# Kernel tuning notes

Hardware: AMD Instinct MI355X
Metric: run time of the kernel (lower is better)

## Reference

```python
import jax, jax.numpy as jnp
import numpy as np

B, L, P = 16, 128, 8192
ALPHA = 2.0            # current_alpha (softness_start)
STEP_PROGRESS = 0.5    # > 0.15 so e_ghost == 0; t_gate = sigmoid(3.0)
PROT_RADII = np.array([1.7, 1.55, 1.52, 1.8], dtype=np.float32)
PROT_EPS = np.array([0.1, 0.1, 0.15, 0.2], dtype=np.float32)
VDW_RADII = np.array([1.7, 1.55, 1.52, 1.8, 1.1, 1.47, 1.75, 1.85, 1.98], dtype=np.float32)
EPSILON = np.array([0.086, 0.17, 0.21, 0.25, 0.015, 0.061, 0.265, 0.32, 0.4], dtype=np.float32)


def setup_inputs() -> dict:
    key = jax.random.key(0)
    ks = jax.random.split(key, 6)
    # positions spread over ~ a binding-pocket-sized box so distances are realistic
    pos_L = jax.random.normal(ks[0], (B, L, 3), jnp.float32) * 8.0
    pos_P = jax.random.normal(ks[1], (B, P, 3), jnp.float32) * 8.0
    q_L = jax.random.normal(ks[2], (B, L), jnp.float32) * 0.3
    q_P = jax.random.normal(ks[3], (B, P), jnp.float32) * 0.3
    x_L = jax.random.uniform(ks[4], (B, L, 9), jnp.float32)
    x_L = x_L / jnp.sum(x_L, axis=-1, keepdims=True)  # type probabilities
    x_P = jax.random.uniform(ks[5], (B, P, 4), jnp.float32)
    x_P = x_P / jnp.sum(x_P, axis=-1, keepdims=True)
    return {
        'pos_L': pos_L, 'pos_P': pos_P, 'q_L': q_L, 'q_P': q_P,
        'x_L': x_L, 'x_P': x_P,
        'vdw_radii': jnp.asarray(VDW_RADII), 'epsilon_tbl': jnp.asarray(EPSILON),
    }


def reference(pos_L, pos_P, q_L, q_P, x_L, x_P, vdw_radii, epsilon_tbl):
    sg = jax.lax.stop_gradient
    # pairwise geometry: diff [B,L,P,3]
    diff = pos_L[:, :, None, :] - pos_P[:, None, :, :]
    dist_sq = jnp.sum(diff * diff, axis=-1)              # [B,L,P]
    dist = jnp.sqrt(dist_sq + 1e-8)
    # mixed vdw radii
    type_probs_L = x_L[..., :9]
    radii_L = type_probs_L @ vdw_radii                    # [B,L]
    radii_P = x_P[..., :4] @ jnp.asarray(PROT_RADII)      # [B,P]
    sigma_ij = radii_L[:, :, None] + radii_P[:, None, :]  # [B,L,P]
    # soft-core distance
    soft_dist = jnp.sqrt(dist_sq + ALPHA * sigma_ij * sigma_ij + 1e-8)
    # electrostatics (dielectric = 4.0), tanh-clamped
    e_elec_raw = 332.06 * q_L[:, :, None] * q_P[:, None, :] / (4.0 * soft_dist)
    e_elec = 200.0 * jnp.tanh(e_elec_raw / 200.0)
    # LJ 12-6 with geometric-mean epsilon
    eps_L = jax.nn.relu(type_probs_L @ epsilon_tbl)       # [B,L]
    eps_P = x_P[..., :4] @ jnp.asarray(PROT_EPS)          # [B,P]
    eps_ij = jnp.sqrt(eps_L[:, :, None] * eps_P[:, None, :] + 1e-8)
    ratio = jnp.minimum(sigma_ij / (soft_dist + 1e-8), 5.0)
    ratio6 = ratio ** 6
    ratio12 = ratio6 * ratio6
    e_vdw_raw = 4.0 * eps_ij * (ratio12 - ratio6)
    e_pos = 500.0 * jnp.tanh(jax.nn.relu(e_vdw_raw) / 500.0)
    e_neg = -10.0 * jnp.tanh(jax.nn.relu(-e_vdw_raw) / 10.0)
    e_vdw_grad = e_pos + e_neg
    # smooth 12 A cutoff
    dist_mask = jax.nn.sigmoid((12.0 - dist) * 2.0)
    e_soft = jnp.sum((e_elec + e_vdw_grad) * dist_mask, axis=(1, 2))  # [B]
    # hydrophobic surface attraction (carbon-carbon)
    mask_cc = type_probs_L[..., 0][:, :, None] * x_P[..., 0][:, None, :]
    hsa_term = 1.0 / (1.0 + (dist / 4.0) ** 4)
    e_hsa = jnp.sum(-0.5 * mask_cc * hsa_term * dist_mask, axis=(1, 2))
    # Pauli repulsion, gated by step progress
    t_gate = jax.nn.sigmoid(jnp.float32((STEP_PROGRESS - 0.2) * 10.0))
    overlap = jax.nn.relu(sigma_ij * 0.6 - dist)
    e_pauli = t_gate * 100.0 * jnp.sum(overlap * overlap, axis=(1, 2))
    # e_ghost = 0 since STEP_PROGRESS >= 0.15
    e_ghost = jnp.zeros_like(e_pauli)
    e_raw = e_soft + 5.0 * e_hsa + e_pauli + e_ghost
    e_raw = jnp.nan_to_num(e_raw, nan=0.0)
    # logging quantities (detached in the original)
    log_vdw = jnp.clip(sg(e_vdw_raw), -10.0, 500.0)
    log_soft_core = jnp.sum((sg(e_elec) + log_vdw) * sg(dist_mask), axis=(1, 2))
    e_soft_log = jnp.clip(log_soft_core + 5.0 * sg(e_hsa), -500.0, 5000.0)
    e_hard_log = jnp.minimum(sg(e_pauli + e_ghost), 10000.0)
    log_energy_val = jnp.minimum(e_soft_log + e_hard_log, 1000000.0)
    return e_raw, e_hard_log, jnp.float32(ALPHA), log_energy_val
```

## Files before the change

### kernel.cpp

```cpp
#include <hip/hip_runtime.h>
#include <math.h>

#define NB 16
#define NL 128
#define NP 8192
#define CHUNKS 32
#define THREADS 256
#define LSPLIT 4
#define LHALF (NL / LSPLIT)
#define LPAIR (LHALF / 2)

typedef float v2 __attribute__((ext_vector_type(2)));

__device__ __forceinline__ float fexp2(float x) { return __builtin_amdgcn_exp2f(x); }
__device__ __forceinline__ float frcp(float x)  { return __builtin_amdgcn_rcpf(x); }
__device__ __forceinline__ float frsq(float x)  { return __builtin_amdgcn_rsqf(x); }
__device__ __forceinline__ float fsqrt_(float x){ return __builtin_amdgcn_sqrtf(x); }
__device__ __forceinline__ v2 vfma(v2 a, v2 b, v2 c) { return __builtin_elementwise_fma(a, b, c); }

__global__ __launch_bounds__(THREADS) void physics_main(
    const float* __restrict__ pos_L, const float* __restrict__ pos_P,
    const float* __restrict__ q_L,   const float* __restrict__ q_P,
    const float* __restrict__ x_L,   const float* __restrict__ x_P,
    const float* __restrict__ vdw_radii, const float* __restrict__ eps_tbl,
    float* __restrict__ partial)
{
    const int b     = blockIdx.y;
    const int chunk = blockIdx.x;
    const int z     = blockIdx.z;
    const int tid   = threadIdx.x;

    __shared__ float4 lig[LPAIR][3];
    __shared__ float2 lig3[LPAIR];
    __shared__ float red[4][3];

    if (tid < LHALF) {
        const int base = b * NL + z * LHALF + tid;
        float px = pos_L[base * 3 + 0];
        float py = pos_L[base * 3 + 1];
        float pz = pos_L[base * 3 + 2];
        float aq = 83.015f * q_L[base];
        float rad = 0.0f, ep = 0.0f;
        #pragma unroll
        for (int j = 0; j < 9; ++j) {
            float v = x_L[base * 9 + j];
            rad = fmaf(v, vdw_radii[j], rad);
            ep  = fmaf(v, eps_tbl[j],  ep);
        }
        float se4 = 4.0f * fsqrt_(fmaxf(ep, 0.0f));
        float x0  = x_L[base * 9 + 0];
        const int i = tid >> 1, s = tid & 1;
        float* L = (float*)lig;
        L[i * 12 + 0 + s] = px;
        L[i * 12 + 2 + s] = py;
        L[i * 12 + 4 + s] = pz;
        L[i * 12 + 6 + s] = aq;
        L[i * 12 + 8 + s] = rad;
        L[i * 12 + 10 + s] = se4;
        ((float*)lig3)[i * 2 + s] = x0;
    }
    __syncthreads();

    const int p  = chunk * THREADS + tid;
    const int pb = b * NP + p;
    const float ppx = pos_P[pb * 3 + 0];
    const float ppy = pos_P[pb * 3 + 1];
    const float ppz = pos_P[pb * 3 + 2];
    const float qP  = q_P[pb];
    const float4 xp = ((const float4*)x_P)[pb];
    const float rP  = 1.7f * xp.x + 1.55f * xp.y + 1.52f * xp.z + 1.8f * xp.w;
    const float epP = 0.1f * xp.x + 0.10f * xp.y + 0.15f * xp.z + 0.2f * xp.w;
    const float seP = fsqrt_(epP);
    const float xP0 = xp.x;

    v2 s1v = (v2)0.0f, s2v = (v2)0.0f, s3v = (v2)0.0f;
    const v2 onev = (v2)1.0f;
    const v2 C1 = (v2)(-8.3333333e-6f);
    const v2 C2 = (v2)(8.3333333e-11f);

    #pragma unroll 4
    for (int i = 0; i < LPAIR; ++i) {
        const float4 t0 = lig[i][0];
        const float4 t1 = lig[i][1];
        const float4 t2 = lig[i][2];
        const float2 t3 = lig3[i];

        v2 lx; lx.x = t0.x; lx.y = t0.y;
        v2 ly; ly.x = t0.z; ly.y = t0.w;
        v2 lz; lz.x = t1.x; lz.y = t1.y;
        v2 laq; laq.x = t1.z; laq.y = t1.w;
        v2 lrad; lrad.x = t2.x; lrad.y = t2.y;
        v2 lse; lse.x = t2.z; lse.y = t2.w;
        v2 lx0; lx0.x = t3.x; lx0.y = t3.y;

        v2 dx = lx - ppx, dy = ly - ppy, dz = lz - ppz;
        v2 ds = vfma(dx, dx, vfma(dy, dy, vfma(dz, dz, (v2)1e-8f)));
        v2 dist; dist.x = fsqrt_(ds.x); dist.y = fsqrt_(ds.y);

        v2 sigma = lrad + rP;
        v2 sigsq = sigma * sigma;
        v2 sd2 = vfma(sigsq, (v2)2.0f, ds);
        v2 inv; inv.x = frsq(sd2.x); inv.y = frsq(sd2.y);

        v2 v = laq * (qP * inv);
        v2 w = v * v;
        v2 pf = vfma(w, vfma(w, C2, C1), onev);
        v2 e_elec = v * pf;

        v2 r2 = sigsq * (inv * inv);
        v2 r6 = r2 * r2 * r2;
        v2 t126 = vfma(r6, r6, -r6);
        v2 ev = (lse * seP) * t126;
        v2 addend = e_elec + ev;

        v2 m = vfma(dist, (v2)2.8853901f, (v2)(-34.624681f));
        v2 A; A.x = fexp2(m.x); A.y = fexp2(m.y);
        A = A + onev;
        v2 tq = ds * 0.0625f;
        v2 Bh = vfma(tq, tq, onev);
        v2 AB = A * Bh;
        v2 r; r.x = frcp(AB.x); r.y = frcp(AB.y);
        v2 dm = Bh * r;

        s1v = vfma(addend, dm, s1v);
        s2v = vfma(lx0, r, s2v);
        v2 ov = __builtin_elementwise_max(vfma(sigma, (v2)0.6f, -dist), (v2)0.0f);
        s3v = vfma(ov, ov, s3v);
    }

    float s1 = s1v.x + s1v.y;
    float s2 = (s2v.x + s2v.y) * xP0;
    float s3 = s3v.x + s3v.y;

    #pragma unroll
    for (int off = 32; off > 0; off >>= 1) {
        s1 += __shfl_down(s1, off);
        s2 += __shfl_down(s2, off);
        s3 += __shfl_down(s3, off);
    }
    const int lane = tid & 63;
    const int wid  = tid >> 6;
    if (lane == 0) {
        red[wid][0] = s1; red[wid][1] = s2; red[wid][2] = s3;
    }
    __syncthreads();
    if (tid == 0) {
        float r0 = red[0][0] + red[1][0] + red[2][0] + red[3][0];
        float r1 = red[0][1] + red[1][1] + red[2][1] + red[3][1];
        float r2_ = red[0][2] + red[1][2] + red[2][2] + red[3][2];
        float* dst = partial + ((size_t)((b * CHUNKS + chunk) * LSPLIT + z)) * 4;
        dst[0] = r0; dst[1] = r1; dst[2] = r2_;
    }
}

__global__ void physics_final(const float* __restrict__ partial, float* __restrict__ out)
{
    const int b = threadIdx.x;
    if (b == 0) out[2 * NB] = 2.0f;
    if (b >= NB) return;
    float s1 = 0.0f, s2 = 0.0f, s3 = 0.0f;
    #pragma unroll 8
    for (int c = 0; c < CHUNKS * LSPLIT; ++c) {
        const float* src = partial + ((size_t)(b * CHUNKS * LSPLIT + c)) * 4;
        s1 += src[0]; s2 += src[1]; s3 += src[2];
    }
    const float TG100 = 95.25741268224334f;
    float e_pauli = TG100 * s3;
    float e_hsa5  = -2.5f * s2;
    float e_raw = s1 + e_hsa5 + e_pauli;
    if (e_raw != e_raw) e_raw = 0.0f;
    float e_hard_log = fminf(e_pauli, 10000.0f);
    float e_soft_log = fminf(fmaxf(s1 + e_hsa5, -500.0f), 5000.0f);
    float log_energy = fminf(e_soft_log + e_hard_log, 1000000.0f);

    out[b]              = e_raw;
    out[NB + b]         = e_hard_log;
    out[2 * NB + 1 + b] = log_energy;
}

extern "C" void kernel_launch(void* const* d_in, const int* in_sizes, int n_in,
                              void* d_out, int out_size, void* d_ws, size_t ws_size,
                              hipStream_t stream)
{
    const float* pos_L = (const float*)d_in[0];
    const float* pos_P = (const float*)d_in[1];
    const float* q_L   = (const float*)d_in[2];
    const float* q_P   = (const float*)d_in[3];
    const float* x_L   = (const float*)d_in[4];
    const float* x_P   = (const float*)d_in[5];
    const float* vdw   = (const float*)d_in[6];
    const float* epst  = (const float*)d_in[7];
    float* out = (float*)d_out;
    float* partial = (float*)d_ws;

    dim3 grid(CHUNKS, NB, LSPLIT);
    physics_main<<<grid, THREADS, 0, stream>>>(pos_L, pos_P, q_L, q_P, x_L, x_P,
                                               vdw, epst, partial);
    physics_final<<<1, 64, 0, stream>>>(partial, out);
}
```

Before: 92.04 us.

## Precompute ligand params in separate kernel and read via uniform global loads

Moves per-ligand parameter preparation into a new lig_prep kernel that writes a packed buffer to workspace. The main kernel then drops its shared-memory staging and __syncthreads, reading ligand data straight from global memory with addresses that are uniform across the block, which the compiler can turn into scalar loads. The final reduction is also parallelised across 16 lanes per batch, using shuffles in place of a serial loop. This adds a third kernel launch and depends on the compiler scalarising the uniform loads.

```diff
diff --git a/kernel.cpp b/kernel.cpp
--- a/kernel.cpp
+++ b/kernel.cpp
@@ -7,8 +7,8 @@
 #define CHUNKS 32
 #define THREADS 256
 #define LSPLIT 4
-#define LHALF (NL / LSPLIT)
-#define LPAIR (LHALF / 2)
+#define LPB 16
+#define NPAIR 64
 
 typedef float v2 __attribute__((ext_vector_type(2)));
 
@@ -18,11 +18,44 @@
 __device__ __forceinline__ float fsqrt_(float x){ return __builtin_amdgcn_sqrtf(x); }
 __device__ __forceinline__ v2 vfma(v2 a, v2 b, v2 c) { return __builtin_elementwise_fma(a, b, c); }
 
+__global__ __launch_bounds__(256) void lig_prep(
+    const float* __restrict__ pos_L, const float* __restrict__ q_L,
+    const float* __restrict__ x_L,
+    const float* __restrict__ vdw_radii, const float* __restrict__ eps_tbl,
+    float* __restrict__ ligbuf)
+{
+    const int id = blockIdx.x * 256 + threadIdx.x;
+    if (id >= NB * NL) return;
+    const int b = id >> 7, l = id & 127;
+    const int base = b * NL + l;
+    float px = pos_L[base * 3 + 0];
+    float py = pos_L[base * 3 + 1];
+    float pz = pos_L[base * 3 + 2];
+    float aq = 83.015f * q_L[base];
+    float rad = 0.0f, ep = 0.0f;
+    #pragma unroll
+    for (int j = 0; j < 9; ++j) {
+        float v = x_L[base * 9 + j];
+        rad = fmaf(v, vdw_radii[j], rad);
+        ep  = fmaf(v, eps_tbl[j],  ep);
+    }
+    float se4 = 4.0f * fsqrt_(fmaxf(ep, 0.0f));
+    float x0  = x_L[base * 9 + 0];
+    const int pair = l >> 1, s = l & 1;
+    float* dst = ligbuf + ((size_t)(b * NPAIR + pair)) * 16;
+    dst[ 0 + s] = px;
+    dst[ 2 + s] = py;
+    dst[ 4 + s] = pz;
+    dst[ 6 + s] = aq;
+    dst[ 8 + s] = rad;
+    dst[10 + s] = se4;
+    dst[12 + s] = x0;
+    dst[14 + s] = 0.0f;
+}
+
 __global__ __launch_bounds__(THREADS) void physics_main(
-    const float* __restrict__ pos_L, const float* __restrict__ pos_P,
-    const float* __restrict__ q_L,   const float* __restrict__ q_P,
-    const float* __restrict__ x_L,   const float* __restrict__ x_P,
-    const float* __restrict__ vdw_radii, const float* __restrict__ eps_tbl,
+    const float* __restrict__ pos_P, const float* __restrict__ q_P,
+    const float* __restrict__ x_P,   const float* __restrict__ ligbuf,
     float* __restrict__ partial)
 {
     const int b     = blockIdx.y;
@@ -30,39 +63,9 @@
     const int z     = blockIdx.z;
     const int tid   = threadIdx.x;
 
-    __shared__ float4 lig[LPAIR][3];
-    __shared__ float2 lig3[LPAIR];
     __shared__ float red[4][3];
 
-    if (tid < LHALF) {
-        const int base = b * NL + z * LHALF + tid;
-        float px = pos_L[base * 3 + 0];
-        float py = pos_L[base * 3 + 1];
-        float pz = pos_L[base * 3 + 2];
-        float aq = 83.015f * q_L[base];
-        float rad = 0.0f, ep = 0.0f;
-        #pragma unroll
-        for (int j = 0; j < 9; ++j) {
-            float v = x_L[base * 9 + j];
-            rad = fmaf(v, vdw_radii[j], rad);
-            ep  = fmaf(v, eps_tbl[j],  ep);
-        }
-        float se4 = 4.0f * fsqrt_(fmaxf(ep, 0.0f));
-        float x0  = x_L[base * 9 + 0];
-        const int i = tid >> 1, s = tid & 1;
-        float* L = (float*)lig;
-        L[i * 12 + 0 + s] = px;
-        L[i * 12 + 2 + s] = py;
-        L[i * 12 + 4 + s] = pz;
-        L[i * 12 + 6 + s] = aq;
-        L[i * 12 + 8 + s] = rad;
-        L[i * 12 + 10 + s] = se4;
-        ((float*)lig3)[i * 2 + s] = x0;
-    }
-    __syncthreads();
-
-    const int p  = chunk * THREADS + tid;
-    const int pb = b * NP + p;
+    const int pb = b * NP + chunk * THREADS + tid;
     const float ppx = pos_P[pb * 3 + 0];
     const float ppy = pos_P[pb * 3 + 1];
     const float ppz = pos_P[pb * 3 + 2];
@@ -73,50 +76,55 @@
     const float seP = fsqrt_(epP);
     const float xP0 = xp.x;
 
-    v2 s1v = (v2)0.0f, s2v = (v2)0.0f, s3v = (v2)0.0f;
+    v2 ppx2; ppx2.x = ppx; ppx2.y = ppx;
+    v2 ppy2; ppy2.x = ppy; ppy2.y = ppy;
+    v2 ppz2; ppz2.x = ppz; ppz2.y = ppz;
+    v2 qP2;  qP2.x  = qP;  qP2.y  = qP;
+    v2 rP2;  rP2.x  = rP;  rP2.y  = rP;
+    v2 seP2; seP2.x = seP; seP2.y = seP;
     const v2 onev = (v2)1.0f;
     const v2 C1 = (v2)(-8.3333333e-6f);
     const v2 C2 = (v2)(8.3333333e-11f);
+    const v2 K1 = (v2)(2.8853901f);
+    const v2 K2 = (v2)(-34.624681f);
+    const v2 KQ = (v2)(0.0625f);
+    const v2 KO = (v2)(0.6f);
+
+    v2 s1v = (v2)0.0f, s2v = (v2)0.0f, s3v = (v2)0.0f;
+
+    const float* lp = ligbuf + ((size_t)(b * NPAIR + z * LPB)) * 16;
 
     #pragma unroll 4
-    for (int i = 0; i < LPAIR; ++i) {
-        const float4 t0 = lig[i][0];
-        const float4 t1 = lig[i][1];
-        const float4 t2 = lig[i][2];
-        const float2 t3 = lig3[i];
-
-        v2 lx; lx.x = t0.x; lx.y = t0.y;
-        v2 ly; ly.x = t0.z; ly.y = t0.w;
-        v2 lz; lz.x = t1.x; lz.y = t1.y;
-        v2 laq; laq.x = t1.z; laq.y = t1.w;
-        v2 lrad; lrad.x = t2.x; lrad.y = t2.y;
-        v2 lse; lse.x = t2.z; lse.y = t2.w;
-        v2 lx0; lx0.x = t3.x; lx0.y = t3.y;
-
-        v2 dx = lx - ppx, dy = ly - ppy, dz = lz - ppz;
+    for (int i = 0; i < LPB; ++i) {
+        const v2* L = (const v2*)(lp + i * 16);
+        v2 lx = L[0], ly = L[1], lz = L[2], laq = L[3];
+        v2 lrad = L[4], lse = L[5], lx0 = L[6];
+
+        v2 dx = lx - ppx2, dy = ly - ppy2, dz = lz - ppz2;
         v2 ds = vfma(dx, dx, vfma(dy, dy, vfma(dz, dz, (v2)1e-8f)));
         v2 dist; dist.x = fsqrt_(ds.x); dist.y = fsqrt_(ds.y);
 
-        v2 sigma = lrad + rP;
+        v2 sigma = lrad + rP2;
         v2 sigsq = sigma * sigma;
         v2 sd2 = vfma(sigsq, (v2)2.0f, ds);
         v2 inv; inv.x = frsq(sd2.x); inv.y = frsq(sd2.y);
 
-        v2 v = laq * (qP * inv);
+        v2 v = (laq * qP2) * inv;
         v2 w = v * v;
         v2 pf = vfma(w, vfma(w, C2, C1), onev);
         v2 e_elec = v * pf;
 
-        v2 r2 = sigsq * (inv * inv);
+        v2 inv2 = inv * inv;
+        v2 r2 = sigsq * inv2;
         v2 r6 = r2 * r2 * r2;
         v2 t126 = vfma(r6, r6, -r6);
-        v2 ev = (lse * seP) * t126;
+        v2 ev = (lse * seP2) * t126;
         v2 addend = e_elec + ev;
 
-        v2 m = vfma(dist, (v2)2.8853901f, (v2)(-34.624681f));
+        v2 m = vfma(dist, K1, K2);
         v2 A; A.x = fexp2(m.x); A.y = fexp2(m.y);
         A = A + onev;
-        v2 tq = ds * 0.0625f;
+        v2 tq = ds * KQ;
         v2 Bh = vfma(tq, tq, onev);
         v2 AB = A * Bh;
         v2 r; r.x = frcp(AB.x); r.y = frcp(AB.y);
@@ -124,7 +132,7 @@
 
         s1v = vfma(addend, dm, s1v);
         s2v = vfma(lx0, r, s2v);
-        v2 ov = __builtin_elementwise_max(vfma(sigma, (v2)0.6f, -dist), (v2)0.0f);
+        v2 ov = __builtin_elementwise_max(vfma(sigma, KO, -dist), (v2)0.0f);
         s3v = vfma(ov, ov, s3v);
     }
 
@@ -140,9 +148,7 @@
     }
     const int lane = tid & 63;
     const int wid  = tid >> 6;
-    if (lane == 0) {
-        red[wid][0] = s1; red[wid][1] = s2; red[wid][2] = s3;
-    }
+    if (lane == 0) { red[wid][0] = s1; red[wid][1] = s2; red[wid][2] = s3; }
     __syncthreads();
     if (tid == 0) {
         float r0 = red[0][0] + red[1][0] + red[2][0] + red[3][0];
@@ -153,29 +159,39 @@
     }
 }
 
-__global__ void physics_final(const float* __restrict__ partial, float* __restrict__ out)
-{
-    const int b = threadIdx.x;
-    if (b == 0) out[2 * NB] = 2.0f;
-    if (b >= NB) return;
+__global__ __launch_bounds__(256) void physics_final(
+    const float* __restrict__ partial, float* __restrict__ out)
+{
+    const int tid = threadIdx.x;
+    if (tid == 0) out[2 * NB] = 2.0f;
+    const int b = tid >> 4;
+    const int j = tid & 15;
     float s1 = 0.0f, s2 = 0.0f, s3 = 0.0f;
-    #pragma unroll 8
-    for (int c = 0; c < CHUNKS * LSPLIT; ++c) {
-        const float* src = partial + ((size_t)(b * CHUNKS * LSPLIT + c)) * 4;
+    const int NPART = CHUNKS * LSPLIT;
+    #pragma unroll
+    for (int k = 0; k < NPART / 16; ++k) {
+        const float* src = partial + ((size_t)(b * NPART + j * (NPART / 16) + k)) * 4;
         s1 += src[0]; s2 += src[1]; s3 += src[2];
     }
-    const float TG100 = 95.25741268224334f;
-    float e_pauli = TG100 * s3;
-    float e_hsa5  = -2.5f * s2;
-    float e_raw = s1 + e_hsa5 + e_pauli;
-    if (e_raw != e_raw) e_raw = 0.0f;
-    float e_hard_log = fminf(e_pauli, 10000.0f);
-    float e_soft_log = fminf(fmaxf(s1 + e_hsa5, -500.0f), 5000.0f);
-    float log_energy = fminf(e_soft_log + e_hard_log, 1000000.0f);
-
-    out[b]              = e_raw;
-    out[NB + b]         = e_hard_log;
-    out[2 * NB + 1 + b] = log_energy;
+    #pragma unroll
+    for (int off = 8; off > 0; off >>= 1) {
+        s1 += __shfl_down(s1, off, 16);
+        s2 += __shfl_down(s2, off, 16);
+        s3 += __shfl_down(s3, off, 16);
+    }
+    if (j == 0) {
+        const float TG100 = 95.25741268224334f;
+        float e_pauli = TG100 * s3;
+        float e_hsa5  = -2.5f * s2;
+        float e_raw = s1 + e_hsa5 + e_pauli;
+        if (e_raw != e_raw) e_raw = 0.0f;
+        float e_hard_log = fminf(e_pauli, 10000.0f);
+        float e_soft_log = fminf(fmaxf(s1 + e_hsa5, -500.0f), 5000.0f);
+        float log_energy = fminf(e_soft_log + e_hard_log, 1000000.0f);
+        out[b]              = e_raw;
+        out[NB + b]         = e_hard_log;
+        out[2 * NB + 1 + b] = log_energy;
+    }
 }
 
 extern "C" void kernel_launch(void* const* d_in, const int* in_sizes, int n_in,
@@ -191,10 +207,12 @@
     const float* vdw   = (const float*)d_in[6];
     const float* epst  = (const float*)d_in[7];
     float* out = (float*)d_out;
-    float* partial = (float*)d_ws;
-
+
+    float* ligbuf  = (float*)d_ws;
+    float* partial = ligbuf + (size_t)NB * NPAIR * 16;
+
+    lig_prep<<<8, 256, 0, stream>>>(pos_L, q_L, x_L, vdw, epst, ligbuf);
     dim3 grid(CHUNKS, NB, LSPLIT);
-    physics_main<<<grid, THREADS, 0, stream>>>(pos_L, pos_P, q_L, q_P, x_L, x_P,
-                                               vdw, epst, partial);
-    physics_final<<<1, 64, 0, stream>>>(partial, out);
-}
+    physics_main<<<grid, THREADS, 0, stream>>>(pos_P, q_P, x_P, ligbuf, partial);
+    physics_final<<<1, 256, 0, stream>>>(partial, out);
+}
```

Result: no change. 91.73 us (-0.3%).
